# Optimization experiments

Measured on AMD Instinct MI355X. Metric: run time of the kernel, lower is better.

Reference implementation:

```python
import jax, jax.numpy as jnp
import numpy as np

HID = 128

def _gru_cell(xt, hx, w_ih, w_hh, b_ih, b_hh):
    # PyTorch GRUCell: gates ordered r, z, n along dim 0 of weights
    gi = xt @ w_ih.T + b_ih          # [n, 3H]
    gh = hx @ w_hh.T + b_hh          # [n, 3H]
    i_r, i_z, i_n = jnp.split(gi, 3, axis=-1)
    h_r, h_z, h_n = jnp.split(gh, 3, axis=-1)
    r = jax.nn.sigmoid(i_r + h_r)
    z = jax.nn.sigmoid(i_z + h_z)
    n_ = jnp.tanh(i_n + r * h_n)
    return (1.0 - z) * n_ + z * hx


def setup_inputs() -> dict:
    key = jax.random.key(0)
    ks = jax.random.split(key, 11)
    n = 32768
    s = 0.05
    return {
        "x": jax.random.normal(ks[0], (n, 1, 28, 28), jnp.float32),
        "w_ih1": jax.random.normal(ks[1], (3 * HID, 28), jnp.float32) * s,
        "w_hh1": jax.random.normal(ks[2], (3 * HID, HID), jnp.float32) * s,
        "b_ih1": jax.random.normal(ks[3], (3 * HID,), jnp.float32) * s,
        "b_hh1": jax.random.normal(ks[4], (3 * HID,), jnp.float32) * s,
        "w_ih2": jax.random.normal(ks[5], (3 * HID, HID), jnp.float32) * s,
        "w_hh2": jax.random.normal(ks[6], (3 * HID, HID), jnp.float32) * s,
        "b_ih2": jax.random.normal(ks[7], (3 * HID,), jnp.float32) * s,
        "b_hh2": jax.random.normal(ks[8], (3 * HID,), jnp.float32) * s,
        "w_out": jax.random.normal(ks[9], (10, HID), jnp.float32) * s,
        "b_out": jax.random.normal(ks[10], (10,), jnp.float32) * s,
    }


def reference(x, w_ih1, w_hh1, b_ih1, b_hh1, w_ih2, w_hh2, b_ih2, b_hh2, w_out, b_out):
    n, c, h, w = x.shape
    xs = x.transpose(0, 2, 3, 1).reshape(n, h, w * c)   # [n, 28, 28]
    xs_t = jnp.swapaxes(xs, 0, 1)                       # [h, n, 28] for scan
    h0 = jnp.zeros((n, HID), x.dtype)

    def step(carry, xt):
        h1, h2 = carry
        h1 = jax.nn.relu(_gru_cell(xt, h1, w_ih1, w_hh1, b_ih1, b_hh1))
        h2 = jax.nn.relu(_gru_cell(h1, h2, w_ih2, w_hh2, b_ih2, b_hh2))
        return (h1, h2), None

    (h1, h2), _ = jax.lax.scan(step, (h0, h0), xs_t)
    return h2 @ w_out.T + b_out                         # [n, 10]
```

## Files before the change

### kernel.cpp

```cpp
#include <hip/hip_runtime.h>

typedef _Float16 f16;
typedef _Float16 f16x8 __attribute__((ext_vector_type(8)));
typedef float f32x4 __attribute__((ext_vector_type(4)));

#define NROWS 32768
#define BR 32
#define TS 28

#define MFMA16(A, B, C) __builtin_amdgcn_mfma_f32_16x16x32_f16((A), (B), (C), 0, 0, 0)

__device__ __forceinline__ f32x4 splat4(float v) { f32x4 r = {v, v, v, v}; return r; }
__device__ __forceinline__ float frcp(float v) { return __builtin_amdgcn_rcpf(v); }
__device__ __forceinline__ float fsig(float v) { return frcp(1.f + __expf(-v)); }
__device__ __forceinline__ float ftanh(float v) {
  float e = __expf(v + v);
  return 1.f - 2.f * frcp(e + 1.f);
}

__global__ void prep_weights(const float* __restrict__ wih1,
                             const float* __restrict__ whh1,
                             const float* __restrict__ wih2,
                             const float* __restrict__ whh2,
                             f16* __restrict__ wsf) {
  const int f = blockIdx.x;
  const int lane = threadIdx.x;
  const float* src;
  int K, nt, kt;
  if (f < 24)       { src = wih1; K = 28;  nt = f;             kt = 0; }
  else if (f < 120) { src = whh1; K = 128; int i = f - 24;  nt = i >> 2; kt = i & 3; }
  else if (f < 216) { src = wih2; K = 128; int i = f - 120; nt = i >> 2; kt = i & 3; }
  else              { src = whh2; K = 128; int i = f - 216; nt = i >> 2; kt = i & 3; }
  const int n  = nt * 16 + (lane & 15);
  const int k0 = kt * 32 + (lane >> 4) * 8;
  f16x8 pack;
#pragma unroll
  for (int i = 0; i < 8; i++) {
    const int k = k0 + i;
    float v = (k < K) ? src[n * K + k] : 0.f;
    pack[i] = (f16)v;
  }
  ((f16x8*)wsf)[f * 64 + lane] = pack;
}

__global__ __launch_bounds__(1024, 4) void gru_main(
    const float* __restrict__ x,
    const float* __restrict__ bih1, const float* __restrict__ bhh1,
    const float* __restrict__ bih2, const float* __restrict__ bhh2,
    const float* __restrict__ wout, const float* __restrict__ bout,
    const f16* __restrict__ wsf,
    float* __restrict__ out) {
  __shared__ __align__(16) f16 h1b[2][BR * 128];
  __shared__ __align__(16) f16 h2b[2][BR * 128];
  __shared__ __align__(16) f16 wshx[24 * 512];
  __shared__ __align__(16) f16 wsh2[96 * 512];

  const int tid  = threadIdx.x;
  const int wid  = tid >> 6;
  const int grp  = wid >> 3;
  const int wv   = wid & 7;
  const int lane = tid & 63;
  const int lr   = lane & 15;
  const int kg   = lane >> 4;
  const int row0 = blockIdx.x * BR;
  const int d    = wv * 16 + lr;
  const int sw   = (lr & 7) << 3;

  const f16x8* wf = (const f16x8*)wsf;

  {
    f16x8* wdx = (f16x8*)wshx;
    if (tid < 512) wdx[1024 + tid] = wf[1024 + tid];
    wdx[tid] = wf[tid];
    f16x8* wd2 = (f16x8*)wsh2;
    const f16x8* ws2 = wf + 120 * 64;
#pragma unroll
    for (int i = 0; i < 6; i++) wd2[tid + 1024 * i] = ws2[tid + 1024 * i];
    unsigned int* z1 = (unsigned int*)&h1b[0][0];
    unsigned int* z2 = (unsigned int*)&h2b[1][0];
    z1[tid] = 0u; z1[tid + 1024] = 0u;
    z2[tid] = 0u; z2[tid + 1024] = 0u;
  }

  const int wbase = grp ? 216 : 24;
  f16x8 Wreg[3][4];
#pragma unroll
  for (int g = 0; g < 3; g++)
#pragma unroll
    for (int kt = 0; kt < 4; kt++)
      Wreg[g][kt] = wf[(wbase + (wv + g * 8) * 4 + kt) * 64 + lane];

  const float* bi = grp ? bih2 : bih1;
  const float* bh = grp ? bhh2 : bhh1;
  const float br_ = bi[d] + bh[d];
  const float bz_ = bi[128 + d] + bh[128 + d];
  const float bin = bi[256 + d];
  const float bhn = bh[256 + d];

  float hs[2][4] = {{0, 0, 0, 0}, {0, 0, 0, 0}};

  const f16x8* wlx = (const f16x8*)wshx;
  const f16x8* wl2 = (const f16x8*)wsh2;

  __syncthreads();

  for (int p = 0; p <= TS; p++) {
    const int cur = p & 1;
    const f16* h1r = h1b[cur];
    f16* h1w = h1b[cur ^ 1];
    const f16* h2r = h2b[cur];
    f16* h2w = h2b[cur ^ 1];

    if (grp == 0) {
      if (p < TS) {
        float4 q[2][2];
#pragma unroll
        for (int rt = 0; rt < 2; rt++) {
          const float* a = x + (size_t)(row0 + rt * 16 + lr) * 784 + p * 28 + kg * 8;
          q[rt][0] = *(const float4*)a;
          float4 zz = {0.f, 0.f, 0.f, 0.f};
          q[rt][1] = zz;
          if (kg < 3) q[rt][1] = *(const float4*)(a + 4);
        }
#pragma unroll
        for (int rt = 0; rt < 2; rt++) {
          f32x4 aR = splat4(br_), aZ = splat4(bz_), aI = splat4(bin), aH = splat4(bhn);
          const int ro = (rt * 16 + lr) * 128;
#pragma unroll
          for (int kt = 0; kt < 4; kt++) {
            f16x8 a1 = *(const f16x8*)&h1r[(ro + kt * 32 + kg * 8) ^ sw];
            aR = MFMA16(a1, Wreg[0][kt], aR);
            aZ = MFMA16(a1, Wreg[1][kt], aZ);
            aH = MFMA16(a1, Wreg[2][kt], aH);
          }
          f16x8 ax;
          ax[0] = (f16)q[rt][0].x; ax[1] = (f16)q[rt][0].y;
          ax[2] = (f16)q[rt][0].z; ax[3] = (f16)q[rt][0].w;
          ax[4] = (f16)q[rt][1].x; ax[5] = (f16)q[rt][1].y;
          ax[6] = (f16)q[rt][1].z; ax[7] = (f16)q[rt][1].w;
          f16x8 u0 = wlx[(wv     ) * 64 + lane];
          f16x8 u1 = wlx[(wv +  8) * 64 + lane];
          f16x8 u2 = wlx[(wv + 16) * 64 + lane];
          aR = MFMA16(ax, u0, aR);
          aZ = MFMA16(ax, u1, aZ);
          aI = MFMA16(ax, u2, aI);
#pragma unroll
          for (int i = 0; i < 4; i++) {
            float rg = fsig(aR[i]);
            float zg = fsig(aZ[i]);
            float nn = ftanh(fmaf(rg, aH[i], aI[i]));
            float hp = hs[rt][i];
            float hn = fmaxf(fmaf(zg, hp - nn, nn), 0.f);
            hs[rt][i] = hn;
            const int rr = rt * 16 + kg * 4 + i;
            h1w[(rr * 128 + d) ^ ((rr & 7) << 3)] = (f16)hn;
          }
        }
      }
    } else {
      if (p >= 1) {
#pragma unroll
        for (int rt = 0; rt < 2; rt++) {
          f32x4 aR = splat4(br_), aZ = splat4(bz_), aI = splat4(bin), aH = splat4(bhn);
          const int ro = (rt * 16 + lr) * 128;
#pragma unroll
          for (int kt = 0; kt < 4; kt++) {
            const int o = (ro + kt * 32 + kg * 8) ^ sw;
            f16x8 a1 = *(const f16x8*)&h1r[o];
            f16x8 a2 = *(const f16x8*)&h2r[o];
            f16x8 u0 = wl2[((wv     ) * 4 + kt) * 64 + lane];
            f16x8 u1 = wl2[((wv +  8) * 4 + kt) * 64 + lane];
            f16x8 u2 = wl2[((wv + 16) * 4 + kt) * 64 + lane];
            aR = MFMA16(a1, u0, aR);
            aZ = MFMA16(a1, u1, aZ);
            aI = MFMA16(a1, u2, aI);
            aR = MFMA16(a2, Wreg[0][kt], aR);
            aZ = MFMA16(a2, Wreg[1][kt], aZ);
            aH = MFMA16(a2, Wreg[2][kt], aH);
          }
#pragma unroll
          for (int i = 0; i < 4; i++) {
            float rg = fsig(aR[i]);
            float zg = fsig(aZ[i]);
            float nn = ftanh(fmaf(rg, aH[i], aI[i]));
            float hp = hs[rt][i];
            float hn = fmaxf(fmaf(zg, hp - nn, nn), 0.f);
            hs[rt][i] = hn;
            const int rr = rt * 16 + kg * 4 + i;
            h2w[(rr * 128 + d) ^ ((rr & 7) << 3)] = (f16)hn;
          }
        }
      }
    }
    __syncthreads();
  }

  const int orow = tid >> 4;
  const int ocol = tid & 15;
  if (orow < BR && ocol < 10) {
    const f16* hb = h2b[1];
    float s = bout[ocol];
#pragma unroll 8
    for (int k = 0; k < 128; k++) {
      float hv = (float)hb[(orow * 128 + k) ^ ((orow & 7) << 3)];
      s = fmaf(hv, wout[ocol * 128 + k], s);
    }
    out[(size_t)(row0 + orow) * 10 + ocol] = s;
  }
}

extern "C" void kernel_launch(void* const* d_in, const int* in_sizes, int n_in,
                              void* d_out, int out_size, void* d_ws, size_t ws_size,
                              hipStream_t stream) {
  const float* x    = (const float*)d_in[0];
  const float* wih1 = (const float*)d_in[1];
  const float* whh1 = (const float*)d_in[2];
  const float* bih1 = (const float*)d_in[3];
  const float* bhh1 = (const float*)d_in[4];
  const float* wih2 = (const float*)d_in[5];
  const float* whh2 = (const float*)d_in[6];
  const float* bih2 = (const float*)d_in[7];
  const float* bhh2 = (const float*)d_in[8];
  const float* wout = (const float*)d_in[9];
  const float* bout = (const float*)d_in[10];
  f16* wsf   = (f16*)d_ws;
  float* out = (float*)d_out;

  prep_weights<<<312, 64, 0, stream>>>(wih1, whh1, wih2, whh2, wsf);
  gru_main<<<NROWS / BR, 1024, 0, stream>>>(x, bih1, bhh1, bih2, bhh2,
                                            wout, bout, wsf, out);
}
```

Measured before the change: 593.0 us.

## Prefetch next timestep's input rows into LDS with async global_load_lds

```diff
diff --git a/kernel.cpp b/kernel.cpp
--- a/kernel.cpp
+++ b/kernel.cpp
@@ -16,6 +16,12 @@
 __device__ __forceinline__ float ftanh(float v) {
   float e = __expf(v + v);
   return 1.f - 2.f * frcp(e + 1.f);
+}
+
+__device__ __forceinline__ void gload_lds16(const float* g, void* l) {
+  __builtin_amdgcn_global_load_lds(
+      (const __attribute__((address_space(1))) void*)g,
+      (__attribute__((address_space(3))) void*)l, 16, 0, 0);
 }
 
 __global__ void prep_weights(const float* __restrict__ wih1,
@@ -54,6 +60,7 @@
   __shared__ __align__(16) f16 h2b[2][BR * 128];
   __shared__ __align__(16) f16 wshx[24 * 512];
   __shared__ __align__(16) f16 wsh2[96 * 512];
+  __shared__ __align__(16) float xbuf[2][BR * 32];
 
   const int tid  = threadIdx.x;
   const int wid  = tid >> 6;
@@ -102,6 +109,18 @@
   const f16x8* wlx = (const f16x8*)wshx;
   const f16x8* wl2 = (const f16x8*)wsh2;
 
+  auto issue_x = [&](int p, int nb) {
+    if (wid < 4) {
+      const int j  = wid * 64 + lane;
+      const int xr = j >> 3;
+      int cs = (j & 7) ^ (xr & 7);
+      cs -= (cs == 7);
+      const float* src = x + (size_t)(row0 + xr) * 784 + p * 28 + cs * 4;
+      gload_lds16(src, (char*)&xbuf[nb][0] + wid * 1024);
+    }
+  };
+
+  issue_x(0, 0);
   __syncthreads();
 
   for (int p = 0; p <= TS; p++) {
@@ -111,17 +130,10 @@
     const f16* h2r = h2b[cur];
     f16* h2w = h2b[cur ^ 1];
 
+    if (p + 1 < TS) issue_x(p + 1, cur ^ 1);
+
     if (grp == 0) {
       if (p < TS) {
-        float4 q[2][2];
-#pragma unroll
-        for (int rt = 0; rt < 2; rt++) {
-          const float* a = x + (size_t)(row0 + rt * 16 + lr) * 784 + p * 28 + kg * 8;
-          q[rt][0] = *(const float4*)a;
-          float4 zz = {0.f, 0.f, 0.f, 0.f};
-          q[rt][1] = zz;
-          if (kg < 3) q[rt][1] = *(const float4*)(a + 4);
-        }
 #pragma unroll
         for (int rt = 0; rt < 2; rt++) {
           f32x4 aR = splat4(br_), aZ = splat4(bz_), aI = splat4(bin), aH = splat4(bhn);
@@ -133,11 +145,14 @@
             aZ = MFMA16(a1, Wreg[1][kt], aZ);
             aH = MFMA16(a1, Wreg[2][kt], aH);
           }
+          const int xr = rt * 16 + lr;
+          const float* xrow = &xbuf[cur][xr * 32];
+          const int xs = xr & 7;
+          float4 xa = *(const float4*)&xrow[((kg * 2    ) ^ xs) * 4];
+          float4 xc = *(const float4*)&xrow[((kg * 2 + 1) ^ xs) * 4];
           f16x8 ax;
-          ax[0] = (f16)q[rt][0].x; ax[1] = (f16)q[rt][0].y;
-          ax[2] = (f16)q[rt][0].z; ax[3] = (f16)q[rt][0].w;
-          ax[4] = (f16)q[rt][1].x; ax[5] = (f16)q[rt][1].y;
-          ax[6] = (f16)q[rt][1].z; ax[7] = (f16)q[rt][1].w;
+          ax[0] = (f16)xa.x; ax[1] = (f16)xa.y; ax[2] = (f16)xa.z; ax[3] = (f16)xa.w;
+          ax[4] = (f16)xc.x; ax[5] = (f16)xc.y; ax[6] = (f16)xc.z; ax[7] = (f16)xc.w;
           f16x8 u0 = wlx[(wv     ) * 64 + lane];
           f16x8 u1 = wlx[(wv +  8) * 64 + lane];
           f16x8 u2 = wlx[(wv + 16) * 64 + lane];
```

Result: faster. 503.8 us (-15.0%).
